# Performance work log

Hardware: AMD Instinct MI355X
Metric: run time of the kernel (lower is better)

## Reference

```python
import jax, jax.numpy as jnp
import numpy as np

N = 50000
E = 1600000
IN, HID, OUT = 32, 64, 64

def setup_inputs() -> dict:
    key = jax.random.key(0)
    ks = jax.random.split(key, 10)
    x1 = jax.random.normal(ks[0], (N, IN), dtype=jnp.float32)
    x2 = jax.random.normal(ks[1], (N, IN), dtype=jnp.float32)
    ei1 = jax.random.randint(ks[2], (2, E), 0, N, dtype=jnp.int64)
    ei2 = jax.random.randint(ks[3], (2, E), 0, N, dtype=jnp.int64)
    s1 = 1.0 / np.sqrt(2 * IN)
    s2 = 1.0 / np.sqrt(2 * HID)
    W1 = jax.random.uniform(ks[4], (2 * IN, HID), jnp.float32, -s1, s1)
    b1 = jax.random.uniform(ks[5], (HID,), jnp.float32, -s1, s1)
    prelu_a = jnp.full((HID,), 0.25, dtype=jnp.float32)  # PReLU per-channel init
    W2 = jax.random.uniform(ks[6], (2 * HID, OUT), jnp.float32, -s2, s2)
    b2 = jax.random.uniform(ks[7], (OUT,), jnp.float32, -s2, s2)
    return {"x1": x1, "edge_index1": ei1, "x2": x2, "edge_index2": ei2,
            "W1": W1, "b1": b1, "prelu_a": prelu_a, "W2": W2, "b2": b2}

def _edge_conv(x, src, dst, W, b, n_nodes):
    # PyG EdgeConv: msg = MLP([x_i, x_j - x_i]), aggr = max over incoming edges
    xi = x[dst]                     # [E, d] target node feats
    xj = x[src]                     # [E, d] source node feats
    msg = jax.nn.relu(jnp.concatenate([xi, xj - xi], axis=-1) @ W + b)  # [E, out]
    agg = jax.ops.segment_max(msg, dst, num_segments=n_nodes)
    return jnp.where(jnp.isfinite(agg), agg, 0.0)  # nodes with no in-edges -> 0

def _prelu(x, a):
    return jnp.where(x >= 0, x, a * x)

def _embed(x, edge_index, W1, b1, prelu_a, W2, b2):
    src, dst = edge_index[0], edge_index[1]
    h = _prelu(_edge_conv(x, src, dst, W1, b1, x.shape[0]), prelu_a)
    return _edge_conv(h, src, dst, W2, b2, x.shape[0])

def reference(x1, edge_index1, x2, edge_index2, W1, b1, prelu_a, W2, b2):
    e1 = _embed(x1, edge_index1, W1, b1, prelu_a, W2, b2)
    e2 = _embed(x2, edge_index2, W1, b1, prelu_a, W2, b2)
    return (e1, e2)
```

## Files before the change

kernel.cpp:

```cpp
#include <hip/hip_runtime.h>
#include <hip/hip_fp16.h>


constexpr int HID   = 64;
constexpr int TILE  = 32;
constexpr int TSH   = 5;
constexpr int CAP   = 2048;
constexpr int MAXNB = 2048;
constexpr int EPT   = 16;
constexpr int CAPN  = 96;

typedef _Float16 half8 __attribute__((ext_vector_type(8)));
typedef float    f32x4 __attribute__((ext_vector_type(4)));

__device__ __forceinline__ unsigned int pkmax(unsigned int a, unsigned int b) {
    unsigned int d;
    asm("v_pk_max_f16 %0, %1, %2" : "=v"(d) : "v"(a), "v"(b));
    return d;
}
__device__ __forceinline__ unsigned int f2hbits(float f) {
    const __half h = __float2half_rn(f);
    return (unsigned int)*reinterpret_cast<const unsigned short*>(&h);
}
__device__ __forceinline__ float h2f(unsigned int b16) {
    const unsigned short b = (unsigned short)b16;
    __half h;
    *reinterpret_cast<unsigned short*>(&h) = b;
    return __half2float(h);
}

struct G {
    const float* x;
    const int*   src;
    const int*   dst;
    int* bcnt;
    unsigned int* bin;
    float*          u;
    unsigned short* vk;
    float*          out;
};

__global__ __launch_bounds__(256) void prep_w_kernel(
    const float* __restrict__ W1, const float* __restrict__ W2,
    _Float16* __restrict__ Wc1, _Float16* __restrict__ Wc2)
{
    const int i = blockIdx.x * 256 + threadIdx.x;
    if (i < 32 * 64) {
        const int k = i >> 6, c = i & 63;
        const float lo = W1[k * 64 + c], hi = W1[(32 + k) * 64 + c];
        Wc1[k * 128 + c]      = (_Float16)(lo - hi);
        Wc1[k * 128 + 64 + c] = (_Float16)hi;
    }
    const int j = i - 32 * 64;
    if (j >= 0 && j < 64 * 64) {
        const int k = j >> 6, c = j & 63;
        const float lo = W2[k * 64 + c], hi = W2[(64 + k) * 64 + c];
        Wc2[k * 128 + c]      = (_Float16)(lo - hi);
        Wc2[k * 128 + 64 + c] = (_Float16)hi;
    }
}

__global__ __launch_bounds__(256) void bin_kernel(G g0, G g1, int E, int NB) {
    const G g = blockIdx.y ? g1 : g0;
    __shared__ int lh[MAXNB];
    __shared__ int lb[MAXNB];
    for (int i = threadIdx.x; i < NB; i += 256) lh[i] = 0;
    __syncthreads();

    const int base = blockIdx.x * 256 * EPT;
    unsigned int rec[EPT];
    int bb[EPT];
    #pragma unroll
    for (int k = 0; k < EPT; ++k) {
        const int i = base + k * 256 + threadIdx.x;
        if (i < E) {
            const int d = g.dst[i];
            const int s = g.src[i];
            rec[k] = ((unsigned int)s << TSH) | (unsigned int)(d & (TILE - 1));
            bb[k]  = d >> TSH;
            atomicAdd(&lh[bb[k]], 1);
        } else bb[k] = -1;
    }
    __syncthreads();
    for (int t = threadIdx.x; t < NB; t += 256) {
        const int c = lh[t];
        lb[t] = c ? atomicAdd(&g.bcnt[t], c) : 0;
        lh[t] = 0;
    }
    __syncthreads();
    #pragma unroll
    for (int k = 0; k < EPT; ++k) {
        if (bb[k] >= 0) {
            const int off = atomicAdd(&lh[bb[k]], 1);
            const int pos = lb[bb[k]] + off;
            if (pos < CAP)
                g.bin[(size_t)bb[k] * CAP + pos] = rec[k];
        }
    }
}

template<int K>
__global__ __launch_bounds__(256) void gemm_mfma_kernel(
    G g0, G g1, const _Float16* __restrict__ Wc,
    const float* __restrict__ bias, int N)
{
    const G g = blockIdx.y ? g1 : g0;
    constexpr int KH = K / 32;
    const int lane = threadIdx.x & 63;
    const int m    = lane & 15;
    const int quad = lane >> 4;
    const int wid  = (blockIdx.x * 256 + threadIdx.x) >> 6;
    const int nW   = (gridDim.x * 256) >> 6;

    half8 bf[8][KH];
    #pragma unroll
    for (int t = 0; t < 8; ++t)
        #pragma unroll
        for (int h = 0; h < KH; ++h)
            #pragma unroll
            for (int j = 0; j < 8; ++j)
                bf[t][h][j] = Wc[(h * 32 + quad * 8 + j) * 128 + t * 16 + m];

    float bv[4];
    #pragma unroll
    for (int t = 0; t < 4; ++t) bv[t] = bias[t * 16 + m];

    const float* __restrict__ inp = (K == 32) ? g.x : g.out;
    const int tiles = (N + 15) / 16;

    for (int tile = wid; tile < tiles; tile += nW) {
        const int nbase = tile * 16;
        const int nodeA = min(nbase + m, N - 1);
        const float4* rp = (const float4*)(inp + (size_t)nodeA * K);

        half8 a[KH];
        #pragma unroll
        for (int h = 0; h < KH; ++h) {
            const float4 f0 = rp[h * 8 + quad * 2];
            const float4 f1 = rp[h * 8 + quad * 2 + 1];
            a[h][0] = (_Float16)f0.x; a[h][1] = (_Float16)f0.y;
            a[h][2] = (_Float16)f0.z; a[h][3] = (_Float16)f0.w;
            a[h][4] = (_Float16)f1.x; a[h][5] = (_Float16)f1.y;
            a[h][6] = (_Float16)f1.z; a[h][7] = (_Float16)f1.w;
        }

        f32x4 acc[8];
        #pragma unroll
        for (int t = 0; t < 8; ++t) {
            acc[t] = (f32x4){0.f, 0.f, 0.f, 0.f};
            #pragma unroll
            for (int h = 0; h < KH; ++h)
                acc[t] = __builtin_amdgcn_mfma_f32_16x16x32_f16(
                    a[h], bf[t][h], acc[t], 0, 0, 0);
        }

        #pragma unroll
        for (int r = 0; r < 4; ++r) {
            const int node = nbase + quad * 4 + r;
            if (node < N) {
                float* urow = g.u + (size_t)node * HID;
                #pragma unroll
                for (int t = 0; t < 4; ++t)
                    urow[t * 16 + m] = acc[t][r] + bv[t];
                const unsigned int e0 = f2hbits(acc[4][r]);
                const unsigned int e1 = f2hbits(acc[5][r]);
                const unsigned int e2 = f2hbits(acc[6][r]);
                const unsigned int e3 = f2hbits(acc[7][r]);
                uint2 pack;
                pack.x = (e1 << 16) | e0;
                pack.y = (e3 << 16) | e2;
                ((uint2*)(g.vk + (size_t)node * HID))[m] = pack;
            }
        }
    }
}

__global__ __launch_bounds__(256) void agg_kernel(G g0, G g1, int N, int NB, int two) {
    int b, gi;
    if (two) {
        const int bid = blockIdx.x;
        const int xcd = bid & 7;
        gi = xcd >> 2;
        b  = (bid >> 3) * 4 + (xcd & 3);
    } else { gi = 0; b = blockIdx.x; }
    if (b >= NB) return;
    const G g = gi ? g1 : g0;

    __shared__ int lcnt[TILE];
    __shared__ unsigned short lrec[TILE][CAPN];
    for (int i = threadIdx.x; i < TILE; i += 256) lcnt[i] = 0;
    __syncthreads();

    const int cnt = min(g.bcnt[b], CAP);
    const unsigned int* __restrict__ bp = g.bin + (size_t)b * CAP;
    for (int i = threadIdx.x; i < cnt; i += 256) {
        const unsigned int rec = bp[i];
        const int d = rec & (TILE - 1);
        const int p = atomicAdd(&lcnt[d], 1);
        if (p < CAPN) lrec[d][p] = (unsigned short)(rec >> TSH);
    }
    __syncthreads();

    const int grp = threadIdx.x >> 4;
    const int sub = threadIdx.x & 15;
    const uint2* __restrict__ vk2 = (const uint2*)g.vk;

    #pragma unroll
    for (int half = 0; half < 2; ++half) {
        const int nl = grp + half * 16;
        const int n  = b * TILE + nl;
        if (n >= N) continue;
        const int c = min(lcnt[nl], CAPN);

        unsigned int m0 = 0xFC00FC00u, m1 = 0xFC00FC00u;
        int j = 0;
        for (; j + 8 <= c; j += 8) {
            const uint4 rq = *(const uint4*)(&lrec[nl][j]);
            unsigned int s[8];
            s[0] = rq.x & 0xFFFFu; s[1] = rq.x >> 16;
            s[2] = rq.y & 0xFFFFu; s[3] = rq.y >> 16;
            s[4] = rq.z & 0xFFFFu; s[5] = rq.z >> 16;
            s[6] = rq.w & 0xFFFFu; s[7] = rq.w >> 16;
            uint2 a[8];
            #pragma unroll
            for (int k = 0; k < 8; ++k) a[k] = vk2[(size_t)s[k] * 16 + sub];
            #pragma unroll
            for (int k = 0; k < 8; ++k) {
                m0 = pkmax(m0, a[k].x);
                m1 = pkmax(m1, a[k].y);
            }
        }
        for (; j < c; ++j) {
            const uint2 a = vk2[(size_t)lrec[nl][j] * 16 + sub];
            m0 = pkmax(m0, a.x);
            m1 = pkmax(m1, a.y);
        }

        float mv[4];
        mv[0] = h2f(m0 & 0xFFFFu); mv[1] = h2f(m0 >> 16);
        mv[2] = h2f(m1 & 0xFFFFu); mv[3] = h2f(m1 >> 16);

        const float* __restrict__ urow = g.u + (size_t)n * HID;
        float* __restrict__ orow = g.out + (size_t)n * HID;
        #pragma unroll
        for (int t = 0; t < 4; ++t) {
            float r = 0.f;
            if (c > 0) r = fmaxf(urow[sub + 16 * t] + mv[t], 0.f);
            orow[sub + 16 * t] = r;
        }
    }
}


extern "C" void kernel_launch(void* const* d_in, const int* in_sizes, int n_in,
                              void* d_out, int out_size, void* d_ws, size_t ws_size,
                              hipStream_t stream) {
    const float* x1  = (const float*)d_in[0];
    const int*   ei1 = (const int*)d_in[1];
    const float* x2  = (const float*)d_in[2];
    const int*   ei2 = (const int*)d_in[3];
    const float* W1  = (const float*)d_in[4];
    const float* b1  = (const float*)d_in[5];
    const float* W2  = (const float*)d_in[7];
    const float* b2  = (const float*)d_in[8];

    const int N  = in_sizes[0] / 32;
    const int E  = in_sizes[1] / 2;
    const int NB = (N + TILE - 1) / TILE;
    float* out = (float*)d_out;

    const size_t rowB = (size_t)N * HID * sizeof(float);
    const size_t vkB  = ((size_t)N * HID * 2 + 63) & ~(size_t)63;
    const size_t binB = ((size_t)NB * CAP * sizeof(int) + 63) & ~(size_t)63;
    const size_t nbB  = ((size_t)(NB + 2) * sizeof(int) + 63) & ~(size_t)63;
    const size_t wc1B = ((size_t)32 * 128 * 2 + 63) & ~(size_t)63;
    const size_t wc2B = ((size_t)64 * 128 * 2 + 63) & ~(size_t)63;

    const int bBlk = (E + 256 * EPT - 1) / (256 * EPT);
    const int gBlk = 256;
    const int pBlk = (32 * 64 + 64 * 64 + 255) / 256;
    const int aggBlk2 = ((NB + 3) / 4) * 8;

    _Float16* wc1 = nullptr;
    _Float16* wc2 = nullptr;

    auto run = [&](G ga, G gb, int ny) {
        hipMemsetAsync(ga.bcnt, 0, (size_t)ny * nbB, stream);
        bin_kernel <<<dim3(bBlk, ny), 256, 0, stream>>>(ga, gb, E, NB);
        gemm_mfma_kernel<32><<<dim3(gBlk, ny), 256, 0, stream>>>(ga, gb, wc1, b1, N);
        if (ny == 2) agg_kernel<<<aggBlk2, 256, 0, stream>>>(ga, gb, N, NB, 1);
        else         agg_kernel<<<NB,      256, 0, stream>>>(ga, ga, N, NB, 0);
        gemm_mfma_kernel<64><<<dim3(gBlk, ny), 256, 0, stream>>>(ga, gb, wc2, b2, N);
        if (ny == 2) agg_kernel<<<aggBlk2, 256, 0, stream>>>(ga, gb, N, NB, 1);
        else         agg_kernel<<<NB,      256, 0, stream>>>(ga, ga, N, NB, 0);
    };

    char* ws = (char*)d_ws;
    const size_t needBoth = 2 * rowB + 2 * vkB + 2 * binB + 2 * nbB + wc1B + wc2B;

    if (ws_size >= needBoth) {
        float* u0 = (float*)ws;                  ws += rowB;
        float* u1 = (float*)ws;                  ws += rowB;
        unsigned int* bin0 = (unsigned int*)ws;  ws += binB;
        unsigned int* bin1 = (unsigned int*)ws;  ws += binB;
        unsigned short* vk0 = (unsigned short*)ws;  ws += vkB;
        unsigned short* vk1 = (unsigned short*)ws;  ws += vkB;
        wc1 = (_Float16*)ws;                     ws += wc1B;
        wc2 = (_Float16*)ws;                     ws += wc2B;
        int* bcnt0 = (int*)ws;                   ws += nbB;
        int* bcnt1 = (int*)ws;

        G g0{x1, ei1, ei1 + E, bcnt0, bin0, u0, vk0, out};
        G g1{x2, ei2, ei2 + E, bcnt1, bin1, u1, vk1, out + (size_t)N * HID};
        prep_w_kernel<<<pBlk, 256, 0, stream>>>(W1, W2, wc1, wc2);
        run(g0, g1, 2);
    } else {
        float* u = (float*)ws;                   ws += rowB;
        unsigned int* bin = (unsigned int*)ws;   ws += binB;
        unsigned short* vk = (unsigned short*)ws;  ws += vkB;
        wc1 = (_Float16*)ws;                     ws += wc1B;
        wc2 = (_Float16*)ws;                     ws += wc2B;
        int* bcnt = (int*)ws;

        prep_w_kernel<<<pBlk, 256, 0, stream>>>(W1, W2, wc1, wc2);
        for (int g = 0; g < 2; ++g) {
            const int* ei = g ? ei2 : ei1;
            G gp{g ? x2 : x1, ei, ei + E, bcnt, bin,
                 u, vk, out + (size_t)g * N * HID};
            run(gp, gp, 1);
        }
    }
}
```

Before: 249.2 us.

## Store layer-1 output as fp16, pad agg edge lists with sentinel row, retune sizes

The first aggregation now writes its hidden activations as fp16 into a new buffer, and the second GEMM reads those directly. This halves the intermediate traffic and removes the float-to-half conversions in the GEMM. The aggregation kernel pads each node's neighbour list up to a multiple of 16 using a sentinel row N, whose vk entries are set to -inf by prep_w. That lets the gather loop run a branch-free unrolled-by-16 body with no scalar tail. Bin capacity and edges-per-thread are reduced and the GEMM grid is doubled, which risks overflowing a bin if the degree distribution is skewed.

```diff
diff --git a/kernel.cpp b/kernel.cpp
--- a/kernel.cpp
+++ b/kernel.cpp
@@ -5,9 +5,9 @@
 constexpr int HID   = 64;
 constexpr int TILE  = 32;
 constexpr int TSH   = 5;
-constexpr int CAP   = 2048;
+constexpr int CAP   = 1280;
 constexpr int MAXNB = 2048;
-constexpr int EPT   = 16;
+constexpr int EPT   = 8;
 constexpr int CAPN  = 96;
 
 typedef _Float16 half8 __attribute__((ext_vector_type(8)));
@@ -37,12 +37,14 @@
     unsigned int* bin;
     float*          u;
     unsigned short* vk;
+    _Float16*       h;
     float*          out;
 };
 
 __global__ __launch_bounds__(256) void prep_w_kernel(
     const float* __restrict__ W1, const float* __restrict__ W2,
-    _Float16* __restrict__ Wc1, _Float16* __restrict__ Wc2)
+    _Float16* __restrict__ Wc1, _Float16* __restrict__ Wc2,
+    unsigned short* __restrict__ vkS0, unsigned short* __restrict__ vkS1, int N)
 {
     const int i = blockIdx.x * 256 + threadIdx.x;
     if (i < 32 * 64) {
@@ -57,6 +59,11 @@
         const float lo = W2[k * 64 + c], hi = W2[(64 + k) * 64 + c];
         Wc2[k * 128 + c]      = (_Float16)(lo - hi);
         Wc2[k * 128 + 64 + c] = (_Float16)hi;
+    }
+    const int q = i - (32 * 64 + 64 * 64);
+    if (q >= 0 && q < 2 * HID) {
+        if (q < HID) vkS0[(size_t)N * HID + q]       = 0xFC00u;
+        else         vkS1[(size_t)N * HID + (q-HID)] = 0xFC00u;
     }
 }
 
@@ -99,7 +106,7 @@
     }
 }
 
-template<int K>
+template<int K, bool IN16>
 __global__ __launch_bounds__(256) void gemm_mfma_kernel(
     G g0, G g1, const _Float16* __restrict__ Wc,
     const float* __restrict__ bias, int N)
@@ -116,32 +123,37 @@
     #pragma unroll
     for (int t = 0; t < 8; ++t)
         #pragma unroll
-        for (int h = 0; h < KH; ++h)
+        for (int hh = 0; hh < KH; ++hh)
             #pragma unroll
             for (int j = 0; j < 8; ++j)
-                bf[t][h][j] = Wc[(h * 32 + quad * 8 + j) * 128 + t * 16 + m];
+                bf[t][hh][j] = Wc[(hh * 32 + quad * 8 + j) * 128 + t * 16 + m];
 
     float bv[4];
     #pragma unroll
     for (int t = 0; t < 4; ++t) bv[t] = bias[t * 16 + m];
 
-    const float* __restrict__ inp = (K == 32) ? g.x : g.out;
     const int tiles = (N + 15) / 16;
 
     for (int tile = wid; tile < tiles; tile += nW) {
         const int nbase = tile * 16;
         const int nodeA = min(nbase + m, N - 1);
-        const float4* rp = (const float4*)(inp + (size_t)nodeA * K);
 
         half8 a[KH];
-        #pragma unroll
-        for (int h = 0; h < KH; ++h) {
-            const float4 f0 = rp[h * 8 + quad * 2];
-            const float4 f1 = rp[h * 8 + quad * 2 + 1];
-            a[h][0] = (_Float16)f0.x; a[h][1] = (_Float16)f0.y;
-            a[h][2] = (_Float16)f0.z; a[h][3] = (_Float16)f0.w;
-            a[h][4] = (_Float16)f1.x; a[h][5] = (_Float16)f1.y;
-            a[h][6] = (_Float16)f1.z; a[h][7] = (_Float16)f1.w;
+        if constexpr (IN16) {
+            const half8* rp = (const half8*)(g.h + (size_t)nodeA * K);
+            #pragma unroll
+            for (int hh = 0; hh < KH; ++hh) a[hh] = rp[hh * 4 + quad];
+        } else {
+            const float4* rp = (const float4*)(g.x + (size_t)nodeA * K);
+            #pragma unroll
+            for (int hh = 0; hh < KH; ++hh) {
+                const float4 f0 = rp[hh * 8 + quad * 2];
+                const float4 f1 = rp[hh * 8 + quad * 2 + 1];
+                a[hh][0] = (_Float16)f0.x; a[hh][1] = (_Float16)f0.y;
+                a[hh][2] = (_Float16)f0.z; a[hh][3] = (_Float16)f0.w;
+                a[hh][4] = (_Float16)f1.x; a[hh][5] = (_Float16)f1.y;
+                a[hh][6] = (_Float16)f1.z; a[hh][7] = (_Float16)f1.w;
+            }
         }
 
         f32x4 acc[8];
@@ -149,9 +161,9 @@
         for (int t = 0; t < 8; ++t) {
             acc[t] = (f32x4){0.f, 0.f, 0.f, 0.f};
             #pragma unroll
-            for (int h = 0; h < KH; ++h)
+            for (int hh = 0; hh < KH; ++hh)
                 acc[t] = __builtin_amdgcn_mfma_f32_16x16x32_f16(
-                    a[h], bf[t][h], acc[t], 0, 0, 0);
+                    a[hh], bf[t][hh], acc[t], 0, 0, 0);
         }
 
         #pragma unroll
@@ -175,6 +187,7 @@
     }
 }
 
+template<bool OUT16>
 __global__ __launch_bounds__(256) void agg_kernel(G g0, G g1, int N, int NB, int two) {
     int b, gi;
     if (two) {
@@ -187,7 +200,7 @@
     const G g = gi ? g1 : g0;
 
     __shared__ int lcnt[TILE];
-    __shared__ unsigned short lrec[TILE][CAPN];
+    __shared__ alignas(16) unsigned short lrec[TILE][CAPN];
     for (int i = threadIdx.x; i < TILE; i += 256) lcnt[i] = 0;
     __syncthreads();
 
@@ -200,53 +213,66 @@
         if (p < CAPN) lrec[d][p] = (unsigned short)(rec >> TSH);
     }
     __syncthreads();
+    for (int t = threadIdx.x; t < TILE; t += 256) {
+        const int c  = min(lcnt[t], CAPN);
+        const int cp = (c + 15) & ~15;
+        for (int p = c; p < cp; ++p) lrec[t][p] = (unsigned short)N;
+        lcnt[t] = cp;
+    }
+    __syncthreads();
 
     const int grp = threadIdx.x >> 4;
     const int sub = threadIdx.x & 15;
     const uint2* __restrict__ vk2 = (const uint2*)g.vk;
 
     #pragma unroll
-    for (int half = 0; half < 2; ++half) {
-        const int nl = grp + half * 16;
+    for (int i = 0; i < 2; ++i) {
+        const int nl = grp + 16 * i;
         const int n  = b * TILE + nl;
         if (n >= N) continue;
-        const int c = min(lcnt[nl], CAPN);
+        const int cp = lcnt[nl];
 
         unsigned int m0 = 0xFC00FC00u, m1 = 0xFC00FC00u;
-        int j = 0;
-        for (; j + 8 <= c; j += 8) {
-            const uint4 rq = *(const uint4*)(&lrec[nl][j]);
-            unsigned int s[8];
-            s[0] = rq.x & 0xFFFFu; s[1] = rq.x >> 16;
-            s[2] = rq.y & 0xFFFFu; s[3] = rq.y >> 16;
-            s[4] = rq.z & 0xFFFFu; s[5] = rq.z >> 16;
-            s[6] = rq.w & 0xFFFFu; s[7] = rq.w >> 16;
-            uint2 a[8];
-            #pragma unroll
-            for (int k = 0; k < 8; ++k) a[k] = vk2[(size_t)s[k] * 16 + sub];
-            #pragma unroll
-            for (int k = 0; k < 8; ++k) {
+        for (int j = 0; j < cp; j += 16) {
+            const uint4 q0 = *(const uint4*)(&lrec[nl][j]);
+            const uint4 q1 = *(const uint4*)(&lrec[nl][j + 8]);
+            unsigned int s[16];
+            s[0]  = q0.x & 0xFFFFu; s[1]  = q0.x >> 16;
+            s[2]  = q0.y & 0xFFFFu; s[3]  = q0.y >> 16;
+            s[4]  = q0.z & 0xFFFFu; s[5]  = q0.z >> 16;
+            s[6]  = q0.w & 0xFFFFu; s[7]  = q0.w >> 16;
+            s[8]  = q1.x & 0xFFFFu; s[9]  = q1.x >> 16;
+            s[10] = q1.y & 0xFFFFu; s[11] = q1.y >> 16;
+            s[12] = q1.z & 0xFFFFu; s[13] = q1.z >> 16;
+            s[14] = q1.w & 0xFFFFu; s[15] = q1.w >> 16;
+            uint2 a[16];
+            #pragma unroll
+            for (int k = 0; k < 16; ++k) a[k] = vk2[(size_t)s[k] * 16 + sub];
+            #pragma unroll
+            for (int k = 0; k < 16; ++k) {
                 m0 = pkmax(m0, a[k].x);
                 m1 = pkmax(m1, a[k].y);
             }
         }
-        for (; j < c; ++j) {
-            const uint2 a = vk2[(size_t)lrec[nl][j] * 16 + sub];
-            m0 = pkmax(m0, a.x);
-            m1 = pkmax(m1, a.y);
-        }
-
-        float mv[4];
-        mv[0] = h2f(m0 & 0xFFFFu); mv[1] = h2f(m0 >> 16);
-        mv[2] = h2f(m1 & 0xFFFFu); mv[3] = h2f(m1 >> 16);
-
+
+        const bool has = cp > 0;
         const float* __restrict__ urow = g.u + (size_t)n * HID;
-        float* __restrict__ orow = g.out + (size_t)n * HID;
-        #pragma unroll
-        for (int t = 0; t < 4; ++t) {
-            float r = 0.f;
-            if (c > 0) r = fmaxf(urow[sub + 16 * t] + mv[t], 0.f);
-            orow[sub + 16 * t] = r;
+        const float r0 = has ? fmaxf(urow[sub]      + h2f(m0 & 0xFFFFu), 0.f) : 0.f;
+        const float r1 = has ? fmaxf(urow[sub + 16] + h2f(m0 >> 16),     0.f) : 0.f;
+        const float r2 = has ? fmaxf(urow[sub + 32] + h2f(m1 & 0xFFFFu), 0.f) : 0.f;
+        const float r3 = has ? fmaxf(urow[sub + 48] + h2f(m1 >> 16),     0.f) : 0.f;
+        if constexpr (OUT16) {
+            _Float16* hrow = g.h + (size_t)n * HID;
+            hrow[sub]      = (_Float16)r0;
+            hrow[sub + 16] = (_Float16)r1;
+            hrow[sub + 32] = (_Float16)r2;
+            hrow[sub + 48] = (_Float16)r3;
+        } else {
+            float* __restrict__ orow = g.out + (size_t)n * HID;
+            orow[sub]      = r0;
+            orow[sub + 16] = r1;
+            orow[sub + 32] = r2;
+            orow[sub + 48] = r3;
         }
     }
 }
@@ -270,16 +296,18 @@
     float* out = (float*)d_out;
 
     const size_t rowB = (size_t)N * HID * sizeof(float);
-    const size_t vkB  = ((size_t)N * HID * 2 + 63) & ~(size_t)63;
+    const size_t vkB  = ((size_t)(N + 1) * HID * 2 + 63) & ~(size_t)63;
+    const size_t hB   = ((size_t)N * HID * 2 + 63) & ~(size_t)63;
     const size_t binB = ((size_t)NB * CAP * sizeof(int) + 63) & ~(size_t)63;
     const size_t nbB  = ((size_t)(NB + 2) * sizeof(int) + 63) & ~(size_t)63;
     const size_t wc1B = ((size_t)32 * 128 * 2 + 63) & ~(size_t)63;
     const size_t wc2B = ((size_t)64 * 128 * 2 + 63) & ~(size_t)63;
 
     const int bBlk = (E + 256 * EPT - 1) / (256 * EPT);
-    const int gBlk = 256;
-    const int pBlk = (32 * 64 + 64 * 64 + 255) / 256;
+    const int gBlk = 512;
+    const int pBlk = (32 * 64 + 64 * 64 + 2 * HID + 255) / 256;
     const int aggBlk2 = ((NB + 3) / 4) * 8;
+    const int aggBlk1 = NB;
 
     _Float16* wc1 = nullptr;
     _Float16* wc2 = nullptr;
@@ -287,16 +315,17 @@
     auto run = [&](G ga, G gb, int ny) {
         hipMemsetAsync(ga.bcnt, 0, (size_t)ny * nbB, stream);
         bin_kernel <<<dim3(bBlk, ny), 256, 0, stream>>>(ga, gb, E, NB);
-        gemm_mfma_kernel<32><<<dim3(gBlk, ny), 256, 0, stream>>>(ga, gb, wc1, b1, N);
-        if (ny == 2) agg_kernel<<<aggBlk2, 256, 0, stream>>>(ga, gb, N, NB, 1);
-        else         agg_kernel<<<NB,      256, 0, stream>>>(ga, ga, N, NB, 0);
-        gemm_mfma_kernel<64><<<dim3(gBlk, ny), 256, 0, stream>>>(ga, gb, wc2, b2, N);
-        if (ny == 2) agg_kernel<<<aggBlk2, 256, 0, stream>>>(ga, gb, N, NB, 1);
-        else         agg_kernel<<<NB,      256, 0, stream>>>(ga, ga, N, NB, 0);
+        gemm_mfma_kernel<32,false><<<dim3(gBlk, ny), 256, 0, stream>>>(ga, gb, wc1, b1, N);
+        if (ny == 2) agg_kernel<true><<<aggBlk2, 256, 0, stream>>>(ga, gb, N, NB, 1);
+        else         agg_kernel<true><<<aggBlk1, 256, 0, stream>>>(ga, ga, N, NB, 0);
+        gemm_mfma_kernel<64,true><<<dim3(gBlk, ny), 256, 0, stream>>>(ga, gb, wc2, b2, N);
+        if (ny == 2) agg_kernel<false><<<aggBlk2, 256, 0, stream>>>(ga, gb, N, NB, 1);
+        else         agg_kernel<false><<<aggBlk1, 256, 0, stream>>>(ga, ga, N, NB, 0);
     };
 
     char* ws = (char*)d_ws;
-    const size_t needBoth = 2 * rowB + 2 * vkB + 2 * binB + 2 * nbB + wc1B + wc2B;
+    const size_t needBoth =
+        2 * rowB + 2 * binB + 2 * vkB + 2 * hB + wc1B + wc2B + 2 * nbB;
 
     if (ws_size >= needBoth) {
         float* u0 = (float*)ws;                  ws += rowB;
@@ -305,28 +334,31 @@
         unsigned int* bin1 = (unsigned int*)ws;  ws += binB;
         unsigned short* vk0 = (unsigned short*)ws;  ws += vkB;
         unsigned short* vk1 = (unsigned short*)ws;  ws += vkB;
+        _Float16* h0 = (_Float16*)ws;            ws += hB;
+        _Float16* h1 = (_Float16*)ws;            ws += hB;
         wc1 = (_Float16*)ws;                     ws += wc1B;
         wc2 = (_Float16*)ws;                     ws += wc2B;
         int* bcnt0 = (int*)ws;                   ws += nbB;
         int* bcnt1 = (int*)ws;
 
-        G g0{x1, ei1, ei1 + E, bcnt0, bin0, u0, vk0, out};
-        G g1{x2, ei2, ei2 + E, bcnt1, bin1, u1, vk1, out + (size_t)N * HID};
-        prep_w_kernel<<<pBlk, 256, 0, stream>>>(W1, W2, wc1, wc2);
+        G g0{x1, ei1, ei1 + E, bcnt0, bin0, u0, vk0, h0, out};
+        G g1{x2, ei2, ei2 + E, bcnt1, bin1, u1, vk1, h1, out + (size_t)N * HID};
+        prep_w_kernel<<<pBlk, 256, 0, stream>>>(W1, W2, wc1, wc2, vk0, vk1, N);
         run(g0, g1, 2);
     } else {
         float* u = (float*)ws;                   ws += rowB;
         unsigned int* bin = (unsigned int*)ws;   ws += binB;
         unsigned short* vk = (unsigned short*)ws;  ws += vkB;
+        _Float16* h = (_Float16*)ws;             ws += hB;
         wc1 = (_Float16*)ws;                     ws += wc1B;
         wc2 = (_Float16*)ws;                     ws += wc2B;
         int* bcnt = (int*)ws;
 
-        prep_w_kernel<<<pBlk, 256, 0, stream>>>(W1, W2, wc1, wc2);
+        prep_w_kernel<<<pBlk, 256, 0, stream>>>(W1, W2, wc1, wc2, vk, vk, N);
         for (int g = 0; g < 2; ++g) {
             const int* ei = g ? ei2 : ei1;
             G gp{g ? x2 : x1, ei, ei + E, bcnt, bin,
-                 u, vk, out + (size_t)g * N * HID};
+                 u, vk, h, out + (size_t)g * N * HID};
             run(gp, gp, 1);
         }
     }
```

After: 268.4 us. 7.7% more time.
